# Kernel optimization log

Hardware: AMD Instinct MI355X
Metric: run time of the kernel (lower is better)

Reference implementation:

```python
import jax, jax.numpy as jnp
import numpy as np

NU, NI, D, NLAYERS, B, E = 100000, 50000, 256, 3, 4096, 5_000_000
N = NU + NI


def _build_graph(seed=0):
    rng = np.random.default_rng(seed)
    u = rng.integers(0, NU, E, dtype=np.int64)
    it = rng.integers(0, NI, E, dtype=np.int64)
    key = np.unique(u * NI + it)  # dedupe interactions like dok_matrix does
    u = (key // NI).astype(np.int32)
    it = (key % NI).astype(np.int32)
    rows = np.concatenate([u, it + NU])
    cols = np.concatenate([it + NU, u])
    deg = np.bincount(rows, minlength=N).astype(np.float32)
    dinv = np.power(deg + 1e-7, -0.5).astype(np.float32)  # D^-0.5 with eps as in source
    vals = (dinv[rows] * dinv[cols]).astype(np.float32)
    return rows.astype(np.int32), cols.astype(np.int32), vals


def setup_inputs() -> dict:
    key = jax.random.key(0)
    k1, k2, k3, k4, k5 = jax.random.split(key, 5)
    rows, cols, vals = _build_graph()
    return {
        "user_emb": jax.random.normal(k1, (NU, D), dtype=jnp.float32) * 0.1,
        "item_emb": jax.random.normal(k2, (NI, D), dtype=jnp.float32) * 0.1,
        "vals": jnp.asarray(vals)[:, None],  # [nnz, 1]
        "rows": jnp.asarray(rows),
        "cols": jnp.asarray(cols),
        "userId": jax.random.randint(k3, (B,), 0, NU, dtype=jnp.int32),
        "itemId": jax.random.randint(k4, (B,), 0, NI, dtype=jnp.int32),
        "neg_itemId": jax.random.randint(k5, (B,), 0, NI, dtype=jnp.int32),
    }


def reference(user_emb, item_emb, vals, rows, cols, userId, itemId, neg_itemId):
    # ego embeddings [N, D]
    emb = jnp.concatenate([user_emb, item_emb], axis=0)
    acc = emb
    for _ in range(NLAYERS):
        # SpMM: out[r] += val * emb[c] over COO edges
        emb = jax.ops.segment_sum(vals * emb[cols], rows, num_segments=N)
        acc = acc + emb
    final = acc / jnp.float32(NLAYERS + 1)  # layer-wise mean
    u_all, i_all = final[:NU], final[NU:]
    u = u_all[userId]
    pos = i_all[itemId]
    neg = i_all[neg_itemId]
    pos_scores = jnp.sum(u * pos, axis=1)
    neg_scores = jnp.sum(u * neg, axis=1)
    u_ego = user_emb[userId]
    pos_ego = item_emb[itemId]
    neg_ego = item_emb[neg_itemId]
    return (pos_scores, neg_scores, u_ego, pos_ego, neg_ego)
```

## Files before the change

### kernel.cpp

```cpp
#include <hip/hip_runtime.h>
#include <hip/hip_bf16.h>
#include <stdint.h>

#define NU_ 100000
#define NI_ 50000
#define NN_ 150000
#define D_ 256
#define D4_ 64
#define DQ_ 64

#define NR_ 256
#define IR_ 196
#define TA_ 4096

typedef unsigned int uint;
typedef unsigned char uchar;


__device__ __forceinline__ float wave_absmax4(float4 a, int lane) {
    float m = fmaxf(fmaxf(fabsf(a.x), fabsf(a.y)), fmaxf(fabsf(a.z), fabsf(a.w)));
#pragma unroll
    for (int off = 32; off; off >>= 1) m = fmaxf(m, __shfl_xor(m, off));
    return m;
}

__device__ __forceinline__ uint pack_q4(float4 v, float qs) {
    int c0 = (int)rintf(v.x * qs) + 128;
    int c1 = (int)rintf(v.y * qs) + 128;
    int c2 = (int)rintf(v.z * qs) + 128;
    int c3 = (int)rintf(v.w * qs) + 128;
    return (uint)c0 | ((uint)c1 << 8) | ((uint)c2 << 16) | ((uint)c3 << 24);
}

__device__ __forceinline__ void edge_accum_q(const int* __restrict__ ca, int p, int end, int sub,
                                             const float* __restrict__ wsrc, float dr,
                                             const uint* __restrict__ src, int lane,
                                             float4& acc, float& svv) {
    for (; p + 8 <= end; p += 8) {
        int c[8]; float w[8]; uint x[8];
#pragma unroll
        for (int k = 0; k < 8; ++k) c[k] = __builtin_amdgcn_readfirstlane(ca[p + k]) - sub;
#pragma unroll
        for (int k = 0; k < 8; ++k) w[k] = wsrc[c[k]];
#pragma unroll
        for (int k = 0; k < 8; ++k) x[k] = src[(size_t)c[k] * DQ_ + lane];
#pragma unroll
        for (int k = 0; k < 8; ++k) {
            float vv = dr * w[k];
            svv += vv;
            acc.x = fmaf(vv, (float)(x[k] & 0xffu), acc.x);
            acc.y = fmaf(vv, (float)((x[k] >> 8) & 0xffu), acc.y);
            acc.z = fmaf(vv, (float)((x[k] >> 16) & 0xffu), acc.z);
            acc.w = fmaf(vv, (float)(x[k] >> 24), acc.w);
        }
    }
    for (; p < end; ++p) {
        int c = __builtin_amdgcn_readfirstlane(ca[p]) - sub;
        float vv = dr * wsrc[c];
        svv += vv;
        uint x = src[(size_t)c * DQ_ + lane];
        acc.x = fmaf(vv, (float)(x & 0xffu), acc.x);
        acc.y = fmaf(vv, (float)((x >> 8) & 0xffu), acc.y);
        acc.z = fmaf(vv, (float)((x >> 16) & 0xffu), acc.z);
        acc.w = fmaf(vv, (float)(x >> 24), acc.w);
    }
}

__device__ __forceinline__ void quant_store(float4 acc, uint* __restrict__ dst, int r, int lane,
                                            float dr, float* __restrict__ st_arr,
                                            float* __restrict__ w_arr) {
    float m = wave_absmax4(acc, lane);
    float qs = (m > 0.f) ? 127.0f / m : 0.0f;
    float st = m * (1.0f / 127.0f);
    dst[(size_t)r * DQ_ + lane] = pack_q4(acc, qs);
    if (lane == 0) { st_arr[r] = st; w_arr[r] = dr * st; }
}

__global__ void build1_kernel(const int* __restrict__ u, const int* __restrict__ ecols,
                              int* __restrict__ up, int* __restrict__ counts,
                              int E, int nbRowptr, int nbHist) {
    int b = blockIdx.x;
    if (b < nbRowptr) {
        int e = b * 256 + threadIdx.x;
        if (e >= E) return;
        int cur = u[e];
        int prev = (e == 0) ? -1 : u[e - 1];
        for (int r = prev + 1; r <= cur; ++r) up[r] = e;
        if (e == E - 1)
            for (int r = cur + 1; r <= NU_; ++r) up[r] = E;
    } else {
        int hb = b - nbRowptr;
        for (int i = hb * 256 + threadIdx.x; i < E; i += nbHist * 256)
            atomicAdd(&counts[ecols[i] - NU_], 1);
    }
}

__global__ void build2_kernel(const int* __restrict__ counts, int* __restrict__ ip,
                              int* __restrict__ bsums, const int* __restrict__ up,
                              float* __restrict__ dinv_u, float* __restrict__ dinv_i,
                              const float* __restrict__ user_emb, uint* __restrict__ Xu0,
                              float* __restrict__ w0u,
                              const float* __restrict__ item_emb, uint* __restrict__ Xi0,
                              float* __restrict__ w0i,
                              float* __restrict__ st_dummy_u, float* __restrict__ st_dummy_i,
                              int nbScan, int nbDu, int nbDi, int nbQU, int nbQI) {
    int b = blockIdx.x;
    int tid = threadIdx.x;
    if (b < nbScan) {
        __shared__ int sh[1024];
        int i = b * 1024 + tid;
        int v = (i < NI_) ? counts[i] : 0;
        sh[tid] = v;
        __syncthreads();
        for (int off = 1; off < 1024; off <<= 1) {
            int t = (tid >= off) ? sh[tid - off] : 0;
            __syncthreads();
            sh[tid] += t;
            __syncthreads();
        }
        if (i < NI_) ip[i] = sh[tid] - v;
        if (tid == 1023) bsums[b] = sh[1023];
        return;
    }
    b -= nbScan;
    if (b < nbDu) {
        int i = b * 1024 + tid;
        if (i < NU_) dinv_u[i] = 1.0f / sqrtf((float)(up[i + 1] - up[i]) + 1e-7f);
        return;
    }
    b -= nbDu;
    if (b < nbDi) {
        int i = b * 1024 + tid;
        if (i < NI_) dinv_i[i] = 1.0f / sqrtf((float)counts[i] + 1e-7f);
        return;
    }
    b -= nbDi;
    int lane = tid & 63;
    int wv = tid >> 6;
    if (b < nbQU) {
        int r = b * 16 + wv;
        if (r >= NU_) return;
        float dr = 1.0f / sqrtf((float)(up[r + 1] - up[r]) + 1e-7f);
        float4 v = ((const float4*)(user_emb + (size_t)r * D_))[lane];
        quant_store(v, Xu0, r, lane, dr, st_dummy_u, w0u);
        return;
    }
    b -= nbQU;
    {
        int r = b * 16 + wv;
        if (r >= NI_) return;
        float dr = 1.0f / sqrtf((float)counts[r] + 1e-7f);
        float4 v = ((const float4*)(item_emb + (size_t)r * D_))[lane];
        quant_store(v, Xi0, r, lane, dr, st_dummy_i, w0i);
    }
}

__global__ void scan_sums(int* __restrict__ bsums, int nb, int* __restrict__ ip) {
    __shared__ int sh[256];
    int tid = threadIdx.x;
    int v = (tid < nb) ? bsums[tid] : 0;
    sh[tid] = v;
    __syncthreads();
    for (int off = 1; off < 256; off <<= 1) {
        int t = (tid >= off) ? sh[tid - off] : 0;
        __syncthreads();
        sh[tid] += t;
        __syncthreads();
    }
    if (tid < nb) bsums[tid] = sh[tid] - v;
    if (tid == 255) ip[NI_] = sh[255];
}

__global__ void scan_add(int* __restrict__ ip, const int* __restrict__ bsums) {
    int i = blockIdx.x * 1024 + threadIdx.x;
    if (i < NI_) ip[i] = ip[i] + bsums[i >> 10];
}

__global__ void rcur_init_kernel(const int* __restrict__ ip, int* __restrict__ rcur) {
    int t = threadIdx.x;
    rcur[t] = ip[t * IR_];
}

__global__ __launch_bounds__(256) void fillA_kernel(
    const int* __restrict__ u_arr, const int* __restrict__ ecols,
    int* __restrict__ rcur, uint* __restrict__ staging, int E)
{
    __shared__ uint vals[TA_];
    __shared__ uchar rng[TA_];
    __shared__ int hist[NR_];
    __shared__ int resv[NR_];
    int tid = threadIdx.x;
    int lo = blockIdx.x * TA_;
    int n = E - lo; if (n > TA_) n = TA_;
    if (tid < NR_) hist[tid] = 0;
    __syncthreads();
    for (int i = tid; i < n; i += 256) {
        int it = ecols[lo + i] - NU_;
        int uu = u_arr[lo + i];
        int r = it / IR_;
        int itl = it - r * IR_;
        vals[i] = (uint)uu | ((uint)itl << 17);
        rng[i] = (uchar)r;
        atomicAdd(&hist[r], 1);
    }
    __syncthreads();
    if (tid < NR_) {
        int c = hist[tid];
        resv[tid] = (c > 0) ? atomicAdd(&rcur[tid], c) : 0;
    }
    __syncthreads();
    if (tid < NR_) hist[tid] = 0;
    __syncthreads();
    for (int i = tid; i < n; i += 256) {
        int r = rng[i];
        int rank = atomicAdd(&hist[r], 1);
        staging[resv[r] + rank] = vals[i];
    }
}

__global__ __launch_bounds__(256) void fillB_kernel(
    const uint* __restrict__ staging, const int* __restrict__ ip, int* __restrict__ icol)
{
    __shared__ int cur[IR_];
    int r = blockIdx.x;
    int tid = threadIdx.x;
    int ibase = r * IR_;
    int iend = ibase + IR_; if (iend > NI_) iend = NI_;
    int nIt = iend - ibase;
    if (tid < nIt) cur[tid] = ip[ibase + tid];
    __syncthreads();
    int lo = ip[ibase];
    int hi = ip[iend];
    for (int p = lo + tid; p < hi; p += 256) {
        uint v = staging[p];
        int uu = (int)(v & 0x1FFFFu);
        int itl = (int)(v >> 17);
        int slot = atomicAdd(&cur[itl], 1);
        icol[slot] = uu;
    }
}

__global__ __launch_bounds__(256) void megaL1_kernel(
    const int* __restrict__ up, const int* __restrict__ ecols,
    const int* __restrict__ ip, const int* __restrict__ icol,
    const float* __restrict__ dinv_u, const float* __restrict__ dinv_i,
    const uint* __restrict__ Xu0, const float* __restrict__ w0u,
    const uint* __restrict__ Xi0, const float* __restrict__ w0i,
    uint* __restrict__ Yu1, float* __restrict__ st1u, float* __restrict__ w1u,
    uint* __restrict__ Yi1, float* __restrict__ st1i, float* __restrict__ w1i,
    const float* __restrict__ user_emb, const float* __restrict__ item_emb,
    const int* __restrict__ uId, const int* __restrict__ iId, const int* __restrict__ nId,
    float* __restrict__ accs, float* __restrict__ out_ego, int Bn, int accBlocks)
{
    int b = blockIdx.x;
    int lane = threadIdx.x & 63;
    int wave = threadIdx.x >> 6;
    if (b < accBlocks) {
        int rowId = b * 4 + wave;
        if (rowId >= 3 * Bn) return;
        int s = rowId / Bn;
        int j = rowId - s * Bn;
        const float* src;
        if (s == 0)      src = user_emb + (size_t)uId[j] * D_;
        else if (s == 1) src = item_emb + (size_t)iId[j] * D_;
        else             src = item_emb + (size_t)nId[j] * D_;
        float4 x = ((const float4*)src)[lane];
        ((float4*)accs)[(size_t)rowId * D4_ + lane] = x;
        ((float4*)out_ego)[(size_t)rowId * D4_ + lane] = x;
        return;
    }
    int row = (b - accBlocks) * 4 + wave;
    if (row >= NN_) return;
    float4 acc = make_float4(0.f, 0.f, 0.f, 0.f);
    float svv = 0.f;
    if (row < NU_) {
        int r = row;
        int p   = __builtin_amdgcn_readfirstlane(up[r]);
        int end = __builtin_amdgcn_readfirstlane(up[r + 1]);
        float dr = dinv_u[r];
        edge_accum_q(ecols, p, end, NU_, w0i, dr, Xi0, lane, acc, svv);
        float c = 128.f * svv;
        acc.x -= c; acc.y -= c; acc.z -= c; acc.w -= c;
        quant_store(acc, Yu1, r, lane, dr, st1u, w1u);
    } else {
        int r = row - NU_;
        int p   = __builtin_amdgcn_readfirstlane(ip[r]);
        int end = __builtin_amdgcn_readfirstlane(ip[r + 1]);
        float dr = dinv_i[r];
        edge_accum_q(icol, p, end, 0, w0u, dr, Xu0, lane, acc, svv);
        float c = 128.f * svv;
        acc.x -= c; acc.y -= c; acc.z -= c; acc.w -= c;
        quant_store(acc, Yi1, r, lane, dr, st1i, w1i);
    }
}

__global__ __launch_bounds__(256) void mega2_kernel(
    const int* __restrict__ up, const int* __restrict__ ecols,
    const int* __restrict__ ip, const int* __restrict__ icol,
    const float* __restrict__ dinv_u, const float* __restrict__ dinv_i,
    const uint* __restrict__ Xu1, const float* __restrict__ st1u, const float* __restrict__ w1u,
    const uint* __restrict__ Xi1, const float* __restrict__ st1i, const float* __restrict__ w1i,
    uint* __restrict__ Yu2, float* __restrict__ st2u, float* __restrict__ w2u,
    uint* __restrict__ Yi2, float* __restrict__ st2i, float* __restrict__ w2i,
    const int* __restrict__ uId, const int* __restrict__ iId, const int* __restrict__ nId,
    float* __restrict__ accs, int Bn, int accBlocks)
{
    int b = blockIdx.x;
    int lane = threadIdx.x & 63;
    int wave = threadIdx.x >> 6;
    if (b < accBlocks) {
        int rowId = b * 4 + wave;
        if (rowId >= 3 * Bn) return;
        int s = rowId / Bn;
        int j = rowId - s * Bn;
        uint x; float st;
        if (s == 0)      { int n = uId[j]; x = Xu1[(size_t)n * DQ_ + lane]; st = st1u[n]; }
        else if (s == 1) { int n = iId[j]; x = Xi1[(size_t)n * DQ_ + lane]; st = st1i[n]; }
        else             { int n = nId[j]; x = Xi1[(size_t)n * DQ_ + lane]; st = st1i[n]; }
        float4* a = (float4*)accs + (size_t)rowId * D4_ + lane;
        float4 t = *a;
        t.x += st * ((float)(x & 0xffu) - 128.f);
        t.y += st * ((float)((x >> 8) & 0xffu) - 128.f);
        t.z += st * ((float)((x >> 16) & 0xffu) - 128.f);
        t.w += st * ((float)(x >> 24) - 128.f);
        *a = t;
        return;
    }
    int row = (b - accBlocks) * 4 + wave;
    if (row >= NN_) return;
    float4 acc = make_float4(0.f, 0.f, 0.f, 0.f);
    float svv = 0.f;
    if (row < NU_) {
        int r = row;
        int p   = __builtin_amdgcn_readfirstlane(up[r]);
        int end = __builtin_amdgcn_readfirstlane(up[r + 1]);
        float dr = dinv_u[r];
        edge_accum_q(ecols, p, end, NU_, w1i, dr, Xi1, lane, acc, svv);
        float c = 128.f * svv;
        acc.x -= c; acc.y -= c; acc.z -= c; acc.w -= c;
        quant_store(acc, Yu2, r, lane, dr, st2u, w2u);
    } else {
        int r = row - NU_;
        int p   = __builtin_amdgcn_readfirstlane(ip[r]);
        int end = __builtin_amdgcn_readfirstlane(ip[r + 1]);
        float dr = dinv_i[r];
        edge_accum_q(icol, p, end, 0, w1u, dr, Xu1, lane, acc, svv);
        float c = 128.f * svv;
        acc.x -= c; acc.y -= c; acc.z -= c; acc.w -= c;
        quant_store(acc, Yi2, r, lane, dr, st2i, w2i);
    }
}

__global__ __launch_bounds__(256) void sampled3_kernel(
    const int* __restrict__ up, const int* __restrict__ ecols,
    const int* __restrict__ ip, const int* __restrict__ icol,
    const float* __restrict__ dinv_u, const float* __restrict__ dinv_i,
    const uint* __restrict__ Xu2, const float* __restrict__ st2u, const float* __restrict__ w2u,
    const uint* __restrict__ Xi2, const float* __restrict__ st2i, const float* __restrict__ w2i,
    const int* __restrict__ uId, const int* __restrict__ iId, const int* __restrict__ nId,
    float* __restrict__ accs, int Bn)
{
    int lane = threadIdx.x & 63;
    int rowId = blockIdx.x * 4 + (threadIdx.x >> 6);
    if (rowId >= 3 * Bn) return;
    int s = rowId / Bn;
    int j = rowId - s * Bn;
    float4 acc = make_float4(0.f, 0.f, 0.f, 0.f);
    float svv = 0.f;
    uint self; float selfst;
    if (s == 0) {
        int n = uId[j];
        self = Xu2[(size_t)n * DQ_ + lane]; selfst = st2u[n];
        int p   = __builtin_amdgcn_readfirstlane(up[n]);
        int end = __builtin_amdgcn_readfirstlane(up[n + 1]);
        edge_accum_q(ecols, p, end, NU_, w2i, dinv_u[n], Xi2, lane, acc, svv);
    } else {
        int n = (s == 1) ? iId[j] : nId[j];
        self = Xi2[(size_t)n * DQ_ + lane]; selfst = st2i[n];
        int p   = __builtin_amdgcn_readfirstlane(ip[n]);
        int end = __builtin_amdgcn_readfirstlane(ip[n + 1]);
        edge_accum_q(icol, p, end, 0, w2u, dinv_i[n], Xu2, lane, acc, svv);
    }
    float c = 128.f * svv;
    float4* a = (float4*)accs + (size_t)rowId * D4_ + lane;
    float4 t = *a;
    t.x += acc.x - c + selfst * ((float)(self & 0xffu) - 128.f);
    t.y += acc.y - c + selfst * ((float)((self >> 8) & 0xffu) - 128.f);
    t.z += acc.z - c + selfst * ((float)((self >> 16) & 0xffu) - 128.f);
    t.w += acc.w - c + selfst * ((float)(self >> 24) - 128.f);
    *a = t;
}

__global__ void scores_kernel(const float* __restrict__ acc, float* __restrict__ out_pos,
                              float* __restrict__ out_neg, int Bn) {
    int j = blockIdx.x * 4 + (threadIdx.x >> 6);
    int lane = threadIdx.x & 63;
    if (j >= Bn) return;
    const float4* u = (const float4*)acc + (size_t)j * D4_;
    const float4* p = (const float4*)(acc + (size_t)Bn * D_) + (size_t)j * D4_;
    const float4* n = (const float4*)(acc + (size_t)2 * Bn * D_) + (size_t)j * D4_;
    float4 uu = u[lane], pp = p[lane], nn = n[lane];
    float dp = uu.x * pp.x + uu.y * pp.y + uu.z * pp.z + uu.w * pp.w;
    float dn = uu.x * nn.x + uu.y * nn.y + uu.z * nn.z + uu.w * nn.w;
    for (int off = 32; off; off >>= 1) {
        dp += __shfl_xor(dp, off);
        dn += __shfl_xor(dn, off);
    }
    if (lane == 0) {
        out_pos[j] = dp * (1.0f / 16.0f);
        out_neg[j] = dn * (1.0f / 16.0f);
    }
}

extern "C" void kernel_launch(void* const* d_in, const int* in_sizes, int n_in,
                              void* d_out, int out_size, void* d_ws, size_t ws_size,
                              hipStream_t stream) {
    const float* user_emb = (const float*)d_in[0];
    const float* item_emb = (const float*)d_in[1];
    const int*   rows     = (const int*)d_in[3];
    const int*   cols     = (const int*)d_in[4];
    const int*   userId   = (const int*)d_in[5];
    const int*   itemId   = (const int*)d_in[6];
    const int*   negId    = (const int*)d_in[7];
    int nnz = in_sizes[3];
    int E   = nnz / 2;
    int Bn  = in_sizes[5];

    const int* u_arr = rows;
    const int* ecols = cols;

    uint8_t* ws = (uint8_t*)d_ws;
    size_t off = 0;
    auto alloc = [&](size_t bytes) -> void* {
        void* p = ws + off;
        off += (bytes + 255) & ~(size_t)255;
        return p;
    };
    int*   up      = (int*)alloc((size_t)(NU_ + 1) * sizeof(int));
    int*   ip      = (int*)alloc((size_t)(NI_ + 1) * sizeof(int));
    int*   counts  = (int*)alloc((size_t)NI_ * sizeof(int));
    int*   bsums   = (int*)alloc(256 * sizeof(int));
    int*   rcur    = (int*)alloc(NR_ * sizeof(int));
    float* dinv_u  = (float*)alloc((size_t)NU_ * sizeof(float));
    float* dinv_i  = (float*)alloc((size_t)NI_ * sizeof(float));
    int*   icol    = (int*)alloc((size_t)E * sizeof(int));
    uint*  staging = (uint*)alloc((size_t)E * sizeof(uint));
    uint*  XuA     = (uint*)alloc((size_t)NU_ * DQ_ * sizeof(uint));
    uint*  XuB     = (uint*)alloc((size_t)NU_ * DQ_ * sizeof(uint));
    uint*  XiA     = (uint*)alloc((size_t)NI_ * DQ_ * sizeof(uint));
    uint*  XiB     = (uint*)alloc((size_t)NI_ * DQ_ * sizeof(uint));
    float* w0u     = (float*)alloc((size_t)NU_ * sizeof(float));
    float* w0i     = (float*)alloc((size_t)NI_ * sizeof(float));
    float* st0u    = (float*)alloc((size_t)NU_ * sizeof(float));
    float* st0i    = (float*)alloc((size_t)NI_ * sizeof(float));
    float* st1u    = (float*)alloc((size_t)NU_ * sizeof(float));
    float* w1u     = (float*)alloc((size_t)NU_ * sizeof(float));
    float* st1i    = (float*)alloc((size_t)NI_ * sizeof(float));
    float* w1i     = (float*)alloc((size_t)NI_ * sizeof(float));
    float* st2u    = (float*)alloc((size_t)NU_ * sizeof(float));
    float* w2u     = (float*)alloc((size_t)NU_ * sizeof(float));
    float* st2i    = (float*)alloc((size_t)NI_ * sizeof(float));
    float* w2i     = (float*)alloc((size_t)NI_ * sizeof(float));
    float* accs    = (float*)alloc((size_t)3 * Bn * D_ * sizeof(float));

    float* out_pos = (float*)d_out;
    float* out_neg = out_pos + Bn;
    float* out_ego = out_neg + Bn;

    int accBlocks = (3 * Bn + 3) / 4;

    (void)hipMemsetAsync(counts, 0, (size_t)NI_ * sizeof(int), stream);
    int nbRowptr = (E + 255) / 256;
    int nbHist = 2048;
    build1_kernel<<<nbRowptr + nbHist, 256, 0, stream>>>(u_arr, ecols, up, counts, E, nbRowptr, nbHist);

    int nbScan = (NI_ + 1023) / 1024;
    int nbDu   = (NU_ + 1023) / 1024;
    int nbDi   = (NI_ + 1023) / 1024;
    int nbQU   = (NU_ + 15) / 16;
    int nbQI   = (NI_ + 15) / 16;
    build2_kernel<<<nbScan + nbDu + nbDi + nbQU + nbQI, 1024, 0, stream>>>(
        counts, ip, bsums, up, dinv_u, dinv_i,
        user_emb, XuA, w0u, item_emb, XiA, w0i, st0u, st0i,
        nbScan, nbDu, nbDi, nbQU, nbQI);
    scan_sums<<<1, 256, 0, stream>>>(bsums, nbScan, ip);
    scan_add<<<nbScan, 1024, 0, stream>>>(ip, bsums);
    rcur_init_kernel<<<1, 256, 0, stream>>>(ip, rcur);

    fillA_kernel<<<(E + TA_ - 1) / TA_, 256, 0, stream>>>(u_arr, ecols, rcur, staging, E);
    fillB_kernel<<<NR_, 256, 0, stream>>>(staging, ip, icol);

    int spmmBlocks = (NN_ + 3) / 4;
    megaL1_kernel<<<accBlocks + spmmBlocks, 256, 0, stream>>>(
        up, ecols, ip, icol, dinv_u, dinv_i,
        XuA, w0u, XiA, w0i,
        XuB, st1u, w1u, XiB, st1i, w1i,
        user_emb, item_emb, userId, itemId, negId, accs, out_ego, Bn, accBlocks);

    mega2_kernel<<<accBlocks + spmmBlocks, 256, 0, stream>>>(
        up, ecols, ip, icol, dinv_u, dinv_i,
        XuB, st1u, w1u, XiB, st1i, w1i,
        XuA, st2u, w2u, XiA, st2i, w2i,
        userId, itemId, negId, accs, Bn, accBlocks);

    sampled3_kernel<<<accBlocks, 256, 0, stream>>>(
        up, ecols, ip, icol, dinv_u, dinv_i,
        XuA, st2u, w2u, XiA, st2i, w2i,
        userId, itemId, negId, accs, Bn);

    scores_kernel<<<(Bn + 3) / 4, 256, 0, stream>>>(accs, out_pos, out_neg, Bn);
}
```

Measured before the change: 1.029 ms.

## Overlap item CSR build with user layer-1 SpMM and fuse item layers

Splits the combined layer kernels into user- and item-side kernels. The item-transpose fill (fillA) is interleaved as every 16th block inside the user layer-1 SpMM grid, so CSR construction overlaps useful work. A single item kernel then computes item layers 1 and 2 together, since both depend only on user layers 0 and 1. The rcur init is folded into scan_add. This removes launches and a serial build stage, at the cost of more register pressure in the fused item kernel and different block scheduling.

Result: slower. 1.179 ms (+14.6%).

```diff
diff --git a/kernel.cpp b/kernel.cpp
--- a/kernel.cpp
+++ b/kernel.cpp
@@ -12,12 +12,14 @@
 #define NR_ 256
 #define IR_ 196
 #define TA_ 4096
+#define SPMM_U_BLOCKS 25000
+#define SPMM_I_BLOCKS 12500
 
 typedef unsigned int uint;
 typedef unsigned char uchar;
 
 
-__device__ __forceinline__ float wave_absmax4(float4 a, int lane) {
+__device__ __forceinline__ float wave_absmax4(float4 a) {
     float m = fmaxf(fmaxf(fabsf(a.x), fabsf(a.y)), fmaxf(fabsf(a.z), fabsf(a.w)));
 #pragma unroll
     for (int off = 32; off; off >>= 1) m = fmaxf(m, __shfl_xor(m, off));
@@ -32,6 +34,13 @@
     return (uint)c0 | ((uint)c1 << 8) | ((uint)c2 << 16) | ((uint)c3 << 24);
 }
 
+__device__ __forceinline__ void fma_q(float4& acc, float vv, uint x) {
+    acc.x = fmaf(vv, (float)(x & 0xffu), acc.x);
+    acc.y = fmaf(vv, (float)((x >> 8) & 0xffu), acc.y);
+    acc.z = fmaf(vv, (float)((x >> 16) & 0xffu), acc.z);
+    acc.w = fmaf(vv, (float)(x >> 24), acc.w);
+}
+
 __device__ __forceinline__ void edge_accum_q(const int* __restrict__ ca, int p, int end, int sub,
                                              const float* __restrict__ wsrc, float dr,
                                              const uint* __restrict__ src, int lane,
@@ -48,28 +57,21 @@
         for (int k = 0; k < 8; ++k) {
             float vv = dr * w[k];
             svv += vv;
-            acc.x = fmaf(vv, (float)(x[k] & 0xffu), acc.x);
-            acc.y = fmaf(vv, (float)((x[k] >> 8) & 0xffu), acc.y);
-            acc.z = fmaf(vv, (float)((x[k] >> 16) & 0xffu), acc.z);
-            acc.w = fmaf(vv, (float)(x[k] >> 24), acc.w);
+            fma_q(acc, vv, x[k]);
         }
     }
     for (; p < end; ++p) {
         int c = __builtin_amdgcn_readfirstlane(ca[p]) - sub;
         float vv = dr * wsrc[c];
         svv += vv;
-        uint x = src[(size_t)c * DQ_ + lane];
-        acc.x = fmaf(vv, (float)(x & 0xffu), acc.x);
-        acc.y = fmaf(vv, (float)((x >> 8) & 0xffu), acc.y);
-        acc.z = fmaf(vv, (float)((x >> 16) & 0xffu), acc.z);
-        acc.w = fmaf(vv, (float)(x >> 24), acc.w);
+        fma_q(acc, vv, src[(size_t)c * DQ_ + lane]);
     }
 }
 
 __device__ __forceinline__ void quant_store(float4 acc, uint* __restrict__ dst, int r, int lane,
                                             float dr, float* __restrict__ st_arr,
                                             float* __restrict__ w_arr) {
-    float m = wave_absmax4(acc, lane);
+    float m = wave_absmax4(acc);
     float qs = (m > 0.f) ? 127.0f / m : 0.0f;
     float st = m * (1.0f / 127.0f);
     dst[(size_t)r * DQ_ + lane] = pack_q4(acc, qs);
@@ -102,7 +104,7 @@
                               float* __restrict__ w0u,
                               const float* __restrict__ item_emb, uint* __restrict__ Xi0,
                               float* __restrict__ w0i,
-                              float* __restrict__ st_dummy_u, float* __restrict__ st_dummy_i,
+                              float* __restrict__ st0u, float* __restrict__ st0i,
                               int nbScan, int nbDu, int nbDi, int nbQU, int nbQI) {
     int b = blockIdx.x;
     int tid = threadIdx.x;
@@ -142,7 +144,7 @@
         if (r >= NU_) return;
         float dr = 1.0f / sqrtf((float)(up[r + 1] - up[r]) + 1e-7f);
         float4 v = ((const float4*)(user_emb + (size_t)r * D_))[lane];
-        quant_store(v, Xu0, r, lane, dr, st_dummy_u, w0u);
+        quant_store(v, Xu0, r, lane, dr, st0u, w0u);
         return;
     }
     b -= nbQU;
@@ -151,7 +153,7 @@
         if (r >= NI_) return;
         float dr = 1.0f / sqrtf((float)counts[r] + 1e-7f);
         float4 v = ((const float4*)(item_emb + (size_t)r * D_))[lane];
-        quant_store(v, Xi0, r, lane, dr, st_dummy_i, w0i);
+        quant_store(v, Xi0, r, lane, dr, st0i, w0i);
     }
 }
 
@@ -171,51 +173,99 @@
     if (tid == 255) ip[NI_] = sh[255];
 }
 
-__global__ void scan_add(int* __restrict__ ip, const int* __restrict__ bsums) {
+__global__ void scan_add(int* __restrict__ ip, const int* __restrict__ bsums,
+                         int* __restrict__ rcur) {
     int i = blockIdx.x * 1024 + threadIdx.x;
-    if (i < NI_) ip[i] = ip[i] + bsums[i >> 10];
-}
-
-__global__ void rcur_init_kernel(const int* __restrict__ ip, int* __restrict__ rcur) {
-    int t = threadIdx.x;
-    rcur[t] = ip[t * IR_];
-}
-
-__global__ __launch_bounds__(256) void fillA_kernel(
+    if (i < NI_) {
+        int s = ip[i] + bsums[i >> 10];
+        ip[i] = s;
+        int q = i / IR_;
+        if (i == q * IR_) rcur[q] = s;
+    }
+}
+
+__global__ __launch_bounds__(256) void userL1_kernel(
     const int* __restrict__ u_arr, const int* __restrict__ ecols,
-    int* __restrict__ rcur, uint* __restrict__ staging, int E)
+    const int* __restrict__ up, int* __restrict__ rcur, uint* __restrict__ staging,
+    const float* __restrict__ dinv_u, const float* __restrict__ w0i,
+    const uint* __restrict__ Xi0,
+    uint* __restrict__ Yu1, float* __restrict__ st1u, float* __restrict__ w1u,
+    const float* __restrict__ user_emb, const float* __restrict__ item_emb,
+    const int* __restrict__ uId, const int* __restrict__ iId, const int* __restrict__ nId,
+    float* __restrict__ accs, float* __restrict__ out_ego,
+    int E, int Bn, int nfa)
 {
     __shared__ uint vals[TA_];
     __shared__ uchar rng[TA_];
     __shared__ int hist[NR_];
     __shared__ int resv[NR_];
+    int b = blockIdx.x;
     int tid = threadIdx.x;
-    int lo = blockIdx.x * TA_;
-    int n = E - lo; if (n > TA_) n = TA_;
-    if (tid < NR_) hist[tid] = 0;
-    __syncthreads();
-    for (int i = tid; i < n; i += 256) {
-        int it = ecols[lo + i] - NU_;
-        int uu = u_arr[lo + i];
-        int r = it / IR_;
-        int itl = it - r * IR_;
-        vals[i] = (uint)uu | ((uint)itl << 17);
-        rng[i] = (uchar)r;
-        atomicAdd(&hist[r], 1);
-    }
-    __syncthreads();
-    if (tid < NR_) {
-        int c = hist[tid];
-        resv[tid] = (c > 0) ? atomicAdd(&rcur[tid], c) : 0;
-    }
-    __syncthreads();
-    if (tid < NR_) hist[tid] = 0;
-    __syncthreads();
-    for (int i = tid; i < n; i += 256) {
-        int r = rng[i];
-        int rank = atomicAdd(&hist[r], 1);
-        staging[resv[r] + rank] = vals[i];
-    }
+    int lane = tid & 63;
+    int wave = tid >> 6;
+    int region = nfa << 4;
+    int sb;
+    if (b < region) {
+        if ((b & 15) == 15) {
+            int lo = (b >> 4) * TA_;
+            int n = E - lo; if (n > TA_) n = TA_;
+            if (tid < NR_) hist[tid] = 0;
+            __syncthreads();
+            for (int i = tid; i < n; i += 256) {
+                int it = ecols[lo + i] - NU_;
+                int uu = u_arr[lo + i];
+                int r = it / IR_;
+                int itl = it - r * IR_;
+                vals[i] = (uint)uu | ((uint)itl << 17);
+                rng[i] = (uchar)r;
+                atomicAdd(&hist[r], 1);
+            }
+            __syncthreads();
+            if (tid < NR_) {
+                int c = hist[tid];
+                resv[tid] = (c > 0) ? atomicAdd(&rcur[tid], c) : 0;
+            }
+            __syncthreads();
+            if (tid < NR_) hist[tid] = 0;
+            __syncthreads();
+            for (int i = tid; i < n; i += 256) {
+                int r = rng[i];
+                int rank = atomicAdd(&hist[r], 1);
+                staging[resv[r] + rank] = vals[i];
+            }
+            return;
+        }
+        sb = b - (b >> 4);
+    } else {
+        int rank = (b - region) + 15 * nfa;
+        if (rank < SPMM_U_BLOCKS) {
+            sb = rank;
+        } else {
+            int rowId = (rank - SPMM_U_BLOCKS) * 4 + wave;
+            if (rowId >= 3 * Bn) return;
+            int s = rowId / Bn;
+            int j = rowId - s * Bn;
+            const float* src;
+            if (s == 0)      src = user_emb + (size_t)uId[j] * D_;
+            else if (s == 1) src = item_emb + (size_t)iId[j] * D_;
+            else             src = item_emb + (size_t)nId[j] * D_;
+            float4 x = ((const float4*)src)[lane];
+            ((float4*)accs)[(size_t)rowId * D4_ + lane] = x;
+            ((float4*)out_ego)[(size_t)rowId * D4_ + lane] = x;
+            return;
+        }
+    }
+    int r = sb * 4 + wave;
+    if (r >= NU_) return;
+    int p   = __builtin_amdgcn_readfirstlane(up[r]);
+    int end = __builtin_amdgcn_readfirstlane(up[r + 1]);
+    float dr = dinv_u[r];
+    float4 acc = make_float4(0.f, 0.f, 0.f, 0.f);
+    float svv = 0.f;
+    edge_accum_q(ecols, p, end, NU_, w0i, dr, Xi0, lane, acc, svv);
+    float c = 128.f * svv;
+    acc.x -= c; acc.y -= c; acc.z -= c; acc.w -= c;
+    quant_store(acc, Yu1, r, lane, dr, st1u, w1u);
 }
 
 __global__ __launch_bounds__(256) void fillB_kernel(
@@ -240,68 +290,58 @@
     }
 }
 
-__global__ __launch_bounds__(256) void megaL1_kernel(
+__global__ __launch_bounds__(256) void itemL12_kernel(
+    const int* __restrict__ ip, const int* __restrict__ icol,
+    const float* __restrict__ dinv_i,
+    const uint* __restrict__ Xu0, const float* __restrict__ w0u,
+    const uint* __restrict__ Xu1, const float* __restrict__ w1u,
+    uint* __restrict__ Yi1, float* __restrict__ st1i, float* __restrict__ w1i,
+    uint* __restrict__ Yi2, float* __restrict__ st2i, float* __restrict__ w2i)
+{
+    int lane = threadIdx.x & 63;
+    int r = blockIdx.x * 4 + (threadIdx.x >> 6);
+    if (r >= NI_) return;
+    int p   = __builtin_amdgcn_readfirstlane(ip[r]);
+    int end = __builtin_amdgcn_readfirstlane(ip[r + 1]);
+    float dr = dinv_i[r];
+    float4 acc1 = make_float4(0.f, 0.f, 0.f, 0.f);
+    float4 acc2 = make_float4(0.f, 0.f, 0.f, 0.f);
+    float sv1 = 0.f, sv2 = 0.f;
+    for (; p + 4 <= end; p += 4) {
+        int c[4]; float wa[4], wb[4]; uint xa[4], xb[4];
+#pragma unroll
+        for (int k = 0; k < 4; ++k) c[k] = __builtin_amdgcn_readfirstlane(icol[p + k]);
+#pragma unroll
+        for (int k = 0; k < 4; ++k) { wa[k] = w0u[c[k]]; wb[k] = w1u[c[k]]; }
+#pragma unroll
+        for (int k = 0; k < 4; ++k) {
+            xa[k] = Xu0[(size_t)c[k] * DQ_ + lane];
+            xb[k] = Xu1[(size_t)c[k] * DQ_ + lane];
+        }
+#pragma unroll
+        for (int k = 0; k < 4; ++k) {
+            float va = dr * wa[k]; sv1 += va; fma_q(acc1, va, xa[k]);
+            float vb = dr * wb[k]; sv2 += vb; fma_q(acc2, vb, xb[k]);
+        }
+    }
+    for (; p < end; ++p) {
+        int c = __builtin_amdgcn_readfirstlane(icol[p]);
+        float va = dr * w0u[c]; sv1 += va; fma_q(acc1, va, Xu0[(size_t)c * DQ_ + lane]);
+        float vb = dr * w1u[c]; sv2 += vb; fma_q(acc2, vb, Xu1[(size_t)c * DQ_ + lane]);
+    }
+    float c1 = 128.f * sv1, c2 = 128.f * sv2;
+    acc1.x -= c1; acc1.y -= c1; acc1.z -= c1; acc1.w -= c1;
+    acc2.x -= c2; acc2.y -= c2; acc2.z -= c2; acc2.w -= c2;
+    quant_store(acc1, Yi1, r, lane, dr, st1i, w1i);
+    quant_store(acc2, Yi2, r, lane, dr, st2i, w2i);
+}
+
+__global__ __launch_bounds__(256) void userL2_kernel(
     const int* __restrict__ up, const int* __restrict__ ecols,
-    const int* __restrict__ ip, const int* __restrict__ icol,
-    const float* __restrict__ dinv_u, const float* __restrict__ dinv_i,
-    const uint* __restrict__ Xu0, const float* __restrict__ w0u,
-    const uint* __restrict__ Xi0, const float* __restrict__ w0i,
-    uint* __restrict__ Yu1, float* __restrict__ st1u, float* __restrict__ w1u,
-    uint* __restrict__ Yi1, float* __restrict__ st1i, float* __restrict__ w1i,
-    const float* __restrict__ user_emb, const float* __restrict__ item_emb,
-    const int* __restrict__ uId, const int* __restrict__ iId, const int* __restrict__ nId,
-    float* __restrict__ accs, float* __restrict__ out_ego, int Bn, int accBlocks)
-{
-    int b = blockIdx.x;
-    int lane = threadIdx.x & 63;
-    int wave = threadIdx.x >> 6;
-    if (b < accBlocks) {
-        int rowId = b * 4 + wave;
-        if (rowId >= 3 * Bn) return;
-        int s = rowId / Bn;
-        int j = rowId - s * Bn;
-        const float* src;
-        if (s == 0)      src = user_emb + (size_t)uId[j] * D_;
-        else if (s == 1) src = item_emb + (size_t)iId[j] * D_;
-        else             src = item_emb + (size_t)nId[j] * D_;
-        float4 x = ((const float4*)src)[lane];
-        ((float4*)accs)[(size_t)rowId * D4_ + lane] = x;
-        ((float4*)out_ego)[(size_t)rowId * D4_ + lane] = x;
-        return;
-    }
-    int row = (b - accBlocks) * 4 + wave;
-    if (row >= NN_) return;
-    float4 acc = make_float4(0.f, 0.f, 0.f, 0.f);
-    float svv = 0.f;
-    if (row < NU_) {
-        int r = row;
-        int p   = __builtin_amdgcn_readfirstlane(up[r]);
-        int end = __builtin_amdgcn_readfirstlane(up[r + 1]);
-        float dr = dinv_u[r];
-        edge_accum_q(ecols, p, end, NU_, w0i, dr, Xi0, lane, acc, svv);
-        float c = 128.f * svv;
-        acc.x -= c; acc.y -= c; acc.z -= c; acc.w -= c;
-        quant_store(acc, Yu1, r, lane, dr, st1u, w1u);
-    } else {
-        int r = row - NU_;
-        int p   = __builtin_amdgcn_readfirstlane(ip[r]);
-        int end = __builtin_amdgcn_readfirstlane(ip[r + 1]);
-        float dr = dinv_i[r];
-        edge_accum_q(icol, p, end, 0, w0u, dr, Xu0, lane, acc, svv);
-        float c = 128.f * svv;
-        acc.x -= c; acc.y -= c; acc.z -= c; acc.w -= c;
-        quant_store(acc, Yi1, r, lane, dr, st1i, w1i);
-    }
-}
-
-__global__ __launch_bounds__(256) void mega2_kernel(
-    const int* __restrict__ up, const int* __restrict__ ecols,
-    const int* __restrict__ ip, const int* __restrict__ icol,
-    const float* __restrict__ dinv_u, const float* __restrict__ dinv_i,
-    const uint* __restrict__ Xu1, const float* __restrict__ st1u, const float* __restrict__ w1u,
+    const float* __restrict__ dinv_u,
+    const uint* __restrict__ Xu1, const float* __restrict__ st1u,
     const uint* __restrict__ Xi1, const float* __restrict__ st1i, const float* __restrict__ w1i,
     uint* __restrict__ Yu2, float* __restrict__ st2u, float* __restrict__ w2u,
-    uint* __restrict__ Yi2, float* __restrict__ st2i, float* __restrict__ w2i,
     const int* __restrict__ uId, const int* __restrict__ iId, const int* __restrict__ nId,
     float* __restrict__ accs, int Bn, int accBlocks)
 {
@@ -326,29 +366,17 @@
         *a = t;
         return;
     }
-    int row = (b - accBlocks) * 4 + wave;
-    if (row >= NN_) return;
+    int r = (b - accBlocks) * 4 + wave;
+    if (r >= NU_) return;
+    int p   = __builtin_amdgcn_readfirstlane(up[r]);
+    int end = __builtin_amdgcn_readfirstlane(up[r + 1]);
+    float dr = dinv_u[r];
     float4 acc = make_float4(0.f, 0.f, 0.f, 0.f);
     float svv = 0.f;
-    if (row < NU_) {
-        int r = row;
-        int p   = __builtin_amdgcn_readfirstlane(up[r]);
-        int end = __builtin_amdgcn_readfirstlane(up[r + 1]);
-        float dr = dinv_u[r];
-        edge_accum_q(ecols, p, end, NU_, w1i, dr, Xi1, lane, acc, svv);
-        float c = 128.f * svv;
-        acc.x -= c; acc.y -= c; acc.z -= c; acc.w -= c;
-        quant_store(acc, Yu2, r, lane, dr, st2u, w2u);
-    } else {
-        int r = row - NU_;
-        int p   = __builtin_amdgcn_readfirstlane(ip[r]);
-        int end = __builtin_amdgcn_readfirstlane(ip[r + 1]);
-        float dr = dinv_i[r];
-        edge_accum_q(icol, p, end, 0, w1u, dr, Xu1, lane, acc, svv);
-        float c = 128.f * svv;
-        acc.x -= c; acc.y -= c; acc.z -= c; acc.w -= c;
-        quant_store(acc, Yi2, r, lane, dr, st2i, w2i);
-    }
+    edge_accum_q(ecols, p, end, NU_, w1i, dr, Xi1, lane, acc, svv);
+    float c = 128.f * svv;
+    acc.x -= c; acc.y -= c; acc.z -= c; acc.w -= c;
+    quant_store(acc, Yu2, r, lane, dr, st2u, w2u);
 }
 
 __global__ __launch_bounds__(256) void sampled3_kernel(
@@ -484,24 +512,24 @@
         user_emb, XuA, w0u, item_emb, XiA, w0i, st0u, st0i,
         nbScan, nbDu, nbDi, nbQU, nbQI);
     scan_sums<<<1, 256, 0, stream>>>(bsums, nbScan, ip);
-    scan_add<<<nbScan, 1024, 0, stream>>>(ip, bsums);
-    rcur_init_kernel<<<1, 256, 0, stream>>>(ip, rcur);
-
-    fillA_kernel<<<(E + TA_ - 1) / TA_, 256, 0, stream>>>(u_arr, ecols, rcur, staging, E);
+    scan_add<<<nbScan, 1024, 0, stream>>>(ip, bsums, rcur);
+
+    int nfa = (E + TA_ - 1) / TA_;
+    int gridK4 = SPMM_U_BLOCKS + nfa + accBlocks;
+    userL1_kernel<<<gridK4, 256, 0, stream>>>(
+        u_arr, ecols, up, rcur, staging, dinv_u, w0i, XiA,
+        XuB, st1u, w1u,
+        user_emb, item_emb, userId, itemId, negId, accs, out_ego, E, Bn, nfa);
+
     fillB_kernel<<<NR_, 256, 0, stream>>>(staging, ip, icol);
 
-    int spmmBlocks = (NN_ + 3) / 4;
-    megaL1_kernel<<<accBlocks + spmmBlocks, 256, 0, stream>>>(
-        up, ecols, ip, icol, dinv_u, dinv_i,
-        XuA, w0u, XiA, w0i,
-        XuB, st1u, w1u, XiB, st1i, w1i,
-        user_emb, item_emb, userId, itemId, negId, accs, out_ego, Bn, accBlocks);
-
-    mega2_kernel<<<accBlocks + spmmBlocks, 256, 0, stream>>>(
-        up, ecols, ip, icol, dinv_u, dinv_i,
-        XuB, st1u, w1u, XiB, st1i, w1i,
-        XuA, st2u, w2u, XiA, st2i, w2i,
-        userId, itemId, negId, accs, Bn, accBlocks);
+    itemL12_kernel<<<SPMM_I_BLOCKS, 256, 0, stream>>>(
+        ip, icol, dinv_i, XuA, w0u, XuB, w1u,
+        XiB, st1i, w1i, XiA, st2i, w2i);
+
+    userL2_kernel<<<accBlocks + SPMM_U_BLOCKS, 256, 0, stream>>>(
+        up, ecols, dinv_u, XuB, st1u, XiB, st1i, w1i,
+        XuA, st2u, w2u, userId, itemId, negId, accs, Bn, accBlocks);
 
     sampled3_kernel<<<accBlocks, 256, 0, stream>>>(
         up, ecols, ip, icol, dinv_u, dinv_i,
```

## Fuse quantization into fillA, fold rcur init into scan_add, hoist dinv scaling

Applied to the files above, without the earlier changes.

Moves the layer-0 embedding quantization out of build2 and into the fillA scatter kernel as extra blocks, so the quantize work runs alongside the edge bucketing, and reads the precomputed dinv arrays instead of recomputing them. The rcur_init kernel is removed by having scan_add write the bucket start offsets, which saves one launch. In the SpMM edge loops the per-edge multiply by the destination dinv is hoisted out and applied once per row after accumulation. The merged kernel puts both workloads under the 256-thread block shape and shared-memory footprint of the fill code, and row scaling now happens after the sum instead of per edge.

Measured after the change: 1.023 ms. No clear change (-0.6%).

```diff
diff --git a/kernel.cpp b/kernel.cpp
--- a/kernel.cpp
+++ b/kernel.cpp
@@ -17,7 +17,7 @@
 typedef unsigned char uchar;
 
 
-__device__ __forceinline__ float wave_absmax4(float4 a, int lane) {
+__device__ __forceinline__ float wave_absmax4(float4 a) {
     float m = fmaxf(fmaxf(fabsf(a.x), fabsf(a.y)), fmaxf(fabsf(a.z), fabsf(a.w)));
 #pragma unroll
     for (int off = 32; off; off >>= 1) m = fmaxf(m, __shfl_xor(m, off));
@@ -32,10 +32,17 @@
     return (uint)c0 | ((uint)c1 << 8) | ((uint)c2 << 16) | ((uint)c3 << 24);
 }
 
+__device__ __forceinline__ void fma_q(float4& acc, float vv, uint x) {
+    acc.x = fmaf(vv, (float)(x & 0xffu), acc.x);
+    acc.y = fmaf(vv, (float)((x >> 8) & 0xffu), acc.y);
+    acc.z = fmaf(vv, (float)((x >> 16) & 0xffu), acc.z);
+    acc.w = fmaf(vv, (float)(x >> 24), acc.w);
+}
+
 __device__ __forceinline__ void edge_accum_q(const int* __restrict__ ca, int p, int end, int sub,
-                                             const float* __restrict__ wsrc, float dr,
+                                             const float* __restrict__ wsrc,
                                              const uint* __restrict__ src, int lane,
-                                             float4& acc, float& svv) {
+                                             float4& acc, float& sw) {
     for (; p + 8 <= end; p += 8) {
         int c[8]; float w[8]; uint x[8];
 #pragma unroll
@@ -46,30 +53,22 @@
         for (int k = 0; k < 8; ++k) x[k] = src[(size_t)c[k] * DQ_ + lane];
 #pragma unroll
         for (int k = 0; k < 8; ++k) {
-            float vv = dr * w[k];
-            svv += vv;
-            acc.x = fmaf(vv, (float)(x[k] & 0xffu), acc.x);
-            acc.y = fmaf(vv, (float)((x[k] >> 8) & 0xffu), acc.y);
-            acc.z = fmaf(vv, (float)((x[k] >> 16) & 0xffu), acc.z);
-            acc.w = fmaf(vv, (float)(x[k] >> 24), acc.w);
+            sw += w[k];
+            fma_q(acc, w[k], x[k]);
         }
     }
     for (; p < end; ++p) {
         int c = __builtin_amdgcn_readfirstlane(ca[p]) - sub;
-        float vv = dr * wsrc[c];
-        svv += vv;
-        uint x = src[(size_t)c * DQ_ + lane];
-        acc.x = fmaf(vv, (float)(x & 0xffu), acc.x);
-        acc.y = fmaf(vv, (float)((x >> 8) & 0xffu), acc.y);
-        acc.z = fmaf(vv, (float)((x >> 16) & 0xffu), acc.z);
-        acc.w = fmaf(vv, (float)(x >> 24), acc.w);
+        float w = wsrc[c];
+        sw += w;
+        fma_q(acc, w, src[(size_t)c * DQ_ + lane]);
     }
 }
 
 __device__ __forceinline__ void quant_store(float4 acc, uint* __restrict__ dst, int r, int lane,
                                             float dr, float* __restrict__ st_arr,
                                             float* __restrict__ w_arr) {
-    float m = wave_absmax4(acc, lane);
+    float m = wave_absmax4(acc);
     float qs = (m > 0.f) ? 127.0f / m : 0.0f;
     float st = m * (1.0f / 127.0f);
     dst[(size_t)r * DQ_ + lane] = pack_q4(acc, qs);
@@ -98,12 +97,7 @@
 __global__ void build2_kernel(const int* __restrict__ counts, int* __restrict__ ip,
                               int* __restrict__ bsums, const int* __restrict__ up,
                               float* __restrict__ dinv_u, float* __restrict__ dinv_i,
-                              const float* __restrict__ user_emb, uint* __restrict__ Xu0,
-                              float* __restrict__ w0u,
-                              const float* __restrict__ item_emb, uint* __restrict__ Xi0,
-                              float* __restrict__ w0i,
-                              float* __restrict__ st_dummy_u, float* __restrict__ st_dummy_i,
-                              int nbScan, int nbDu, int nbDi, int nbQU, int nbQI) {
+                              int nbScan, int nbDu, int nbDi) {
     int b = blockIdx.x;
     int tid = threadIdx.x;
     if (b < nbScan) {
@@ -129,29 +123,9 @@
         return;
     }
     b -= nbDu;
-    if (b < nbDi) {
+    {
         int i = b * 1024 + tid;
         if (i < NI_) dinv_i[i] = 1.0f / sqrtf((float)counts[i] + 1e-7f);
-        return;
-    }
-    b -= nbDi;
-    int lane = tid & 63;
-    int wv = tid >> 6;
-    if (b < nbQU) {
-        int r = b * 16 + wv;
-        if (r >= NU_) return;
-        float dr = 1.0f / sqrtf((float)(up[r + 1] - up[r]) + 1e-7f);
-        float4 v = ((const float4*)(user_emb + (size_t)r * D_))[lane];
-        quant_store(v, Xu0, r, lane, dr, st_dummy_u, w0u);
-        return;
-    }
-    b -= nbQU;
-    {
-        int r = b * 16 + wv;
-        if (r >= NI_) return;
-        float dr = 1.0f / sqrtf((float)counts[r] + 1e-7f);
-        float4 v = ((const float4*)(item_emb + (size_t)r * D_))[lane];
-        quant_store(v, Xi0, r, lane, dr, st_dummy_i, w0i);
     }
 }
 
@@ -171,50 +145,77 @@
     if (tid == 255) ip[NI_] = sh[255];
 }
 
-__global__ void scan_add(int* __restrict__ ip, const int* __restrict__ bsums) {
+__global__ void scan_add(int* __restrict__ ip, const int* __restrict__ bsums,
+                         int* __restrict__ rcur) {
     int i = blockIdx.x * 1024 + threadIdx.x;
-    if (i < NI_) ip[i] = ip[i] + bsums[i >> 10];
-}
-
-__global__ void rcur_init_kernel(const int* __restrict__ ip, int* __restrict__ rcur) {
-    int t = threadIdx.x;
-    rcur[t] = ip[t * IR_];
-}
-
-__global__ __launch_bounds__(256) void fillA_kernel(
+    if (i < NI_) {
+        int s = ip[i] + bsums[i >> 10];
+        ip[i] = s;
+        int q = i / IR_;
+        if (i == q * IR_) rcur[q] = s;
+    }
+}
+
+__global__ __launch_bounds__(256) void fillA_quant_kernel(
     const int* __restrict__ u_arr, const int* __restrict__ ecols,
-    int* __restrict__ rcur, uint* __restrict__ staging, int E)
+    int* __restrict__ rcur, uint* __restrict__ staging, int E, int nfa,
+    const float* __restrict__ user_emb, const float* __restrict__ item_emb,
+    const float* __restrict__ dinv_u, const float* __restrict__ dinv_i,
+    uint* __restrict__ Xu0, float* __restrict__ st0u, float* __restrict__ w0u,
+    uint* __restrict__ Xi0, float* __restrict__ st0i, float* __restrict__ w0i,
+    int nbQU)
 {
     __shared__ uint vals[TA_];
     __shared__ uchar rng[TA_];
     __shared__ int hist[NR_];
     __shared__ int resv[NR_];
+    int b = blockIdx.x;
     int tid = threadIdx.x;
-    int lo = blockIdx.x * TA_;
-    int n = E - lo; if (n > TA_) n = TA_;
-    if (tid < NR_) hist[tid] = 0;
-    __syncthreads();
-    for (int i = tid; i < n; i += 256) {
-        int it = ecols[lo + i] - NU_;
-        int uu = u_arr[lo + i];
-        int r = it / IR_;
-        int itl = it - r * IR_;
-        vals[i] = (uint)uu | ((uint)itl << 17);
-        rng[i] = (uchar)r;
-        atomicAdd(&hist[r], 1);
-    }
-    __syncthreads();
-    if (tid < NR_) {
-        int c = hist[tid];
-        resv[tid] = (c > 0) ? atomicAdd(&rcur[tid], c) : 0;
-    }
-    __syncthreads();
-    if (tid < NR_) hist[tid] = 0;
-    __syncthreads();
-    for (int i = tid; i < n; i += 256) {
-        int r = rng[i];
-        int rank = atomicAdd(&hist[r], 1);
-        staging[resv[r] + rank] = vals[i];
+    if (b < nfa) {
+        int lo = b * TA_;
+        int n = E - lo; if (n > TA_) n = TA_;
+        if (tid < NR_) hist[tid] = 0;
+        __syncthreads();
+        for (int i = tid; i < n; i += 256) {
+            int it = ecols[lo + i] - NU_;
+            int uu = u_arr[lo + i];
+            int r = it / IR_;
+            int itl = it - r * IR_;
+            vals[i] = (uint)uu | ((uint)itl << 17);
+            rng[i] = (uchar)r;
+            atomicAdd(&hist[r], 1);
+        }
+        __syncthreads();
+        if (tid < NR_) {
+            int c = hist[tid];
+            resv[tid] = (c > 0) ? atomicAdd(&rcur[tid], c) : 0;
+        }
+        __syncthreads();
+        if (tid < NR_) hist[tid] = 0;
+        __syncthreads();
+        for (int i = tid; i < n; i += 256) {
+            int r = rng[i];
+            int rank = atomicAdd(&hist[r], 1);
+            staging[resv[r] + rank] = vals[i];
+        }
+        return;
+    }
+    b -= nfa;
+    int lane = tid & 63;
+    int wv = tid >> 6;
+    if (b < nbQU) {
+        int r = b * 4 + wv;
+        if (r >= NU_) return;
+        float4 v = ((const float4*)(user_emb + (size_t)r * D_))[lane];
+        quant_store(v, Xu0, r, lane, dinv_u[r], st0u, w0u);
+        return;
+    }
+    b -= nbQU;
+    {
+        int r = b * 4 + wv;
+        if (r >= NI_) return;
+        float4 v = ((const float4*)(item_emb + (size_t)r * D_))[lane];
+        quant_store(v, Xi0, r, lane, dinv_i[r], st0i, w0i);
     }
 }
 
@@ -272,24 +273,26 @@
     int row = (b - accBlocks) * 4 + wave;
     if (row >= NN_) return;
     float4 acc = make_float4(0.f, 0.f, 0.f, 0.f);
-    float svv = 0.f;
+    float sw = 0.f;
     if (row < NU_) {
         int r = row;
         int p   = __builtin_amdgcn_readfirstlane(up[r]);
         int end = __builtin_amdgcn_readfirstlane(up[r + 1]);
         float dr = dinv_u[r];
-        edge_accum_q(ecols, p, end, NU_, w0i, dr, Xi0, lane, acc, svv);
-        float c = 128.f * svv;
-        acc.x -= c; acc.y -= c; acc.z -= c; acc.w -= c;
+        edge_accum_q(ecols, p, end, NU_, w0i, Xi0, lane, acc, sw);
+        float c = 128.f * sw;
+        acc.x = dr * (acc.x - c); acc.y = dr * (acc.y - c);
+        acc.z = dr * (acc.z - c); acc.w = dr * (acc.w - c);
         quant_store(acc, Yu1, r, lane, dr, st1u, w1u);
     } else {
         int r = row - NU_;
         int p   = __builtin_amdgcn_readfirstlane(ip[r]);
         int end = __builtin_amdgcn_readfirstlane(ip[r + 1]);
         float dr = dinv_i[r];
-        edge_accum_q(icol, p, end, 0, w0u, dr, Xu0, lane, acc, svv);
-        float c = 128.f * svv;
-        acc.x -= c; acc.y -= c; acc.z -= c; acc.w -= c;
+        edge_accum_q(icol, p, end, 0, w0u, Xu0, lane, acc, sw);
+        float c = 128.f * sw;
+        acc.x = dr * (acc.x - c); acc.y = dr * (acc.y - c);
+        acc.z = dr * (acc.z - c); acc.w = dr * (acc.w - c);
         quant_store(acc, Yi1, r, lane, dr, st1i, w1i);
     }
 }
@@ -329,24 +332,26 @@
     int row = (b - accBlocks) * 4 + wave;
     if (row >= NN_) return;
     float4 acc = make_float4(0.f, 0.f, 0.f, 0.f);
-    float svv = 0.f;
+    float sw = 0.f;
     if (row < NU_) {
         int r = row;
         int p   = __builtin_amdgcn_readfirstlane(up[r]);
         int end = __builtin_amdgcn_readfirstlane(up[r + 1]);
         float dr = dinv_u[r];
-        edge_accum_q(ecols, p, end, NU_, w1i, dr, Xi1, lane, acc, svv);
-        float c = 128.f * svv;
-        acc.x -= c; acc.y -= c; acc.z -= c; acc.w -= c;
+        edge_accum_q(ecols, p, end, NU_, w1i, Xi1, lane, acc, sw);
+        float c = 128.f * sw;
+        acc.x = dr * (acc.x - c); acc.y = dr * (acc.y - c);
+        acc.z = dr * (acc.z - c); acc.w = dr * (acc.w - c);
         quant_store(acc, Yu2, r, lane, dr, st2u, w2u);
     } else {
         int r = row - NU_;
         int p   = __builtin_amdgcn_readfirstlane(ip[r]);
         int end = __builtin_amdgcn_readfirstlane(ip[r + 1]);
         float dr = dinv_i[r];
-        edge_accum_q(icol, p, end, 0, w1u, dr, Xu1, lane, acc, svv);
-        float c = 128.f * svv;
-        acc.x -= c; acc.y -= c; acc.z -= c; acc.w -= c;
+        edge_accum_q(icol, p, end, 0, w1u, Xu1, lane, acc, sw);
+        float c = 128.f * sw;
+        acc.x = dr * (acc.x - c); acc.y = dr * (acc.y - c);
+        acc.z = dr * (acc.z - c); acc.w = dr * (acc.w - c);
         quant_store(acc, Yi2, r, lane, dr, st2i, w2i);
     }
 }
@@ -366,28 +371,30 @@
     int s = rowId / Bn;
     int j = rowId - s * Bn;
     float4 acc = make_float4(0.f, 0.f, 0.f, 0.f);
-    float svv = 0.f;
-    uint self; float selfst;
+    float sw = 0.f;
+    uint self; float selfst; float dr;
     if (s == 0) {
         int n = uId[j];
         self = Xu2[(size_t)n * DQ_ + lane]; selfst = st2u[n];
         int p   = __builtin_amdgcn_readfirstlane(up[n]);
         int end = __builtin_amdgcn_readfirstlane(up[n + 1]);
-        edge_accum_q(ecols, p, end, NU_, w2i, dinv_u[n], Xi2, lane, acc, svv);
+        dr = dinv_u[n];
+        edge_accum_q(ecols, p, end, NU_, w2i, Xi2, lane, acc, sw);
     } else {
         int n = (s == 1) ? iId[j] : nId[j];
         self = Xi2[(size_t)n * DQ_ + lane]; selfst = st2i[n];
         int p   = __builtin_amdgcn_readfirstlane(ip[n]);
         int end = __builtin_amdgcn_readfirstlane(ip[n + 1]);
-        edge_accum_q(icol, p, end, 0, w2u, dinv_i[n], Xu2, lane, acc, svv);
-    }
-    float c = 128.f * svv;
+        dr = dinv_i[n];
+        edge_accum_q(icol, p, end, 0, w2u, Xu2, lane, acc, sw);
+    }
+    float c = 128.f * sw;
     float4* a = (float4*)accs + (size_t)rowId * D4_ + lane;
     float4 t = *a;
-    t.x += acc.x - c + selfst * ((float)(self & 0xffu) - 128.f);
-    t.y += acc.y - c + selfst * ((float)((self >> 8) & 0xffu) - 128.f);
-    t.z += acc.z - c + selfst * ((float)((self >> 16) & 0xffu) - 128.f);
-    t.w += acc.w - c + selfst * ((float)(self >> 24) - 128.f);
+    t.x += dr * (acc.x - c) + selfst * ((float)(self & 0xffu) - 128.f);
+    t.y += dr * (acc.y - c) + selfst * ((float)((self >> 8) & 0xffu) - 128.f);
+    t.z += dr * (acc.z - c) + selfst * ((float)((self >> 16) & 0xffu) - 128.f);
+    t.w += dr * (acc.w - c) + selfst * ((float)(self >> 24) - 128.f);
     *a = t;
 }
 
@@ -477,17 +484,19 @@
     int nbScan = (NI_ + 1023) / 1024;
     int nbDu   = (NU_ + 1023) / 1024;
     int nbDi   = (NI_ + 1023) / 1024;
-    int nbQU   = (NU_ + 15) / 16;
-    int nbQI   = (NI_ + 15) / 16;
-    build2_kernel<<<nbScan + nbDu + nbDi + nbQU + nbQI, 1024, 0, stream>>>(
-        counts, ip, bsums, up, dinv_u, dinv_i,
-        user_emb, XuA, w0u, item_emb, XiA, w0i, st0u, st0i,
-        nbScan, nbDu, nbDi, nbQU, nbQI);
+    build2_kernel<<<nbScan + nbDu + nbDi, 1024, 0, stream>>>(
+        counts, ip, bsums, up, dinv_u, dinv_i, nbScan, nbDu, nbDi);
     scan_sums<<<1, 256, 0, stream>>>(bsums, nbScan, ip);
-    scan_add<<<nbScan, 1024, 0, stream>>>(ip, bsums);
-    rcur_init_kernel<<<1, 256, 0, stream>>>(ip, rcur);
-
-    fillA_kernel<<<(E + TA_ - 1) / TA_, 256, 0, stream>>>(u_arr, ecols, rcur, staging, E);
+    scan_add<<<nbScan, 1024, 0, stream>>>(ip, bsums, rcur);
+
+    int nfa  = (E + TA_ - 1) / TA_;
+    int nbQU = (NU_ + 3) / 4;
+    int nbQI = (NI_ + 3) / 4;
+    fillA_quant_kernel<<<nfa + nbQU + nbQI, 256, 0, stream>>>(
+        u_arr, ecols, rcur, staging, E, nfa,
+        user_emb, item_emb, dinv_u, dinv_i,
+        XuA, st0u, w0u, XiA, st0i, w0i, nbQU);
+
     fillB_kernel<<<NR_, 256, 0, stream>>>(staging, ip, icol);
 
     int spmmBlocks = (NN_ + 3) / 4;
```
